# Performance work log

Hardware: AMD Instinct MI355X
Metric: run time of the kernel (lower is better)

Reference implementation:

```python
import jax, jax.numpy as jnp
import numpy as np

NUM_EMB = 512
EMB_DIM = 64

def conv1d(x, w, b=None, stride=1, padding=0):
    # x: (N,C,L), w: (O,I,K) torch Conv1d layout
    out = jax.lax.conv_general_dilated(x, w, (stride,), [(padding, padding)],
                                       dimension_numbers=('NCH', 'OIH', 'NCH'))
    if b is not None:
        out = out + b[None, :, None]
    return out

def conv_transpose1d(x, w, b, stride, padding):
    # w: (I,O,K) torch ConvTranspose1d layout -> flip kernel, swap I/O
    k = w.shape[2]
    wf = jnp.flip(w, 2).transpose(1, 0, 2)  # (O,I,K)
    pad = k - 1 - padding
    out = jax.lax.conv_general_dilated(x, wf, (1,), [(pad, pad)],
                                       lhs_dilation=(stride,),
                                       dimension_numbers=('NCH', 'OIH', 'NCH'))
    return out + b[None, :, None]

def residual_block(x, w1, w2):
    # ReLU -> conv3(pad1, no bias) -> ReLU -> conv1(no bias), residual add
    h = conv1d(jax.nn.relu(x), w1, None, 1, 1)
    h = conv1d(jax.nn.relu(h), w2, None, 1, 0)
    return x + h

def residual_stack(x, r0_w1, r0_w2, r1_w1, r1_w2):
    x = residual_block(x, r0_w1, r0_w2)
    x = residual_block(x, r1_w1, r1_w2)
    return jax.nn.relu(x)

def vq(z, emb):
    # z: (B, C=64, T); torch VectorQuantizerEMA eval path (decay=0, not training)
    B, C, T = z.shape
    inputs = z.transpose(0, 2, 1)                 # (B,T,C)
    flat = inputs.reshape(-1, C)                  # (B*T, C)
    d = (jnp.sum(flat * flat, axis=1, keepdims=True)
         + jnp.sum(emb * emb, axis=1)
         - 2.0 * flat @ emb.T)                    # (B*T, K)
    idx = jnp.argmin(d, axis=1)
    enc = jax.nn.one_hot(idx, NUM_EMB, dtype=flat.dtype)  # (B*T, K)
    q = (enc @ emb).reshape(B, T, C)
    # straight-through estimator
    q = inputs + jax.lax.stop_gradient(q - inputs)
    return q.transpose(0, 2, 1)                   # (B,C,T)

def reference(x, enc_w1, enc_b1, enc_w2, enc_b2, enc_w3, enc_b3,
              enc_r0_w1, enc_r0_w2, enc_r1_w1, enc_r1_w2,
              prevq_w, prevq_b, emb,
              dec_w1, dec_b1, dec_r0_w1, dec_r0_w2, dec_r1_w1, dec_r1_w2,
              dect1_w, dect1_b, dect2_w, dect2_b):
    # Encoder
    h = jax.nn.relu(conv1d(x, enc_w1, enc_b1, 2, 1))
    h = jax.nn.relu(conv1d(h, enc_w2, enc_b2, 2, 1))
    h = conv1d(h, enc_w3, enc_b3, 1, 1)
    h = residual_stack(h, enc_r0_w1, enc_r0_w2, enc_r1_w1, enc_r1_w2)
    # pre-VQ 1x1 conv
    z = conv1d(h, prevq_w, prevq_b, 1, 0)
    # Vector quantization
    q = vq(z, emb)
    # Decoder
    d = conv1d(q, dec_w1, dec_b1, 1, 1)
    d = residual_stack(d, dec_r0_w1, dec_r0_w2, dec_r1_w1, dec_r1_w2)
    d = jax.nn.relu(conv_transpose1d(d, dect1_w, dect1_b, 2, 1))
    return conv_transpose1d(d, dect2_w, dect2_b, 2, 1)

def setup_inputs() -> dict:
    key = jax.random.key(0)
    ks = jax.random.split(key, 25)
    def n(k, shape, s=0.05):
        return jax.random.normal(k, shape, dtype=jnp.float32) * s
    return {
        'x': jax.random.normal(ks[0], (16, 768, 4096), dtype=jnp.float32),
        'enc_w1': n(ks[1], (32, 768, 4)), 'enc_b1': n(ks[2], (32,)),
        'enc_w2': n(ks[3], (64, 32, 4)), 'enc_b2': n(ks[4], (64,)),
        'enc_w3': n(ks[5], (64, 64, 3)), 'enc_b3': n(ks[6], (64,)),
        'enc_r0_w1': n(ks[7], (32, 64, 3)), 'enc_r0_w2': n(ks[8], (64, 32, 1)),
        'enc_r1_w1': n(ks[9], (32, 64, 3)), 'enc_r1_w2': n(ks[10], (64, 32, 1)),
        'prevq_w': n(ks[11], (64, 64, 1)), 'prevq_b': n(ks[12], (64,)),
        'emb': jax.random.normal(ks[13], (512, 64), dtype=jnp.float32),
        'dec_w1': n(ks[14], (64, 64, 3)), 'dec_b1': n(ks[15], (64,)),
        'dec_r0_w1': n(ks[16], (32, 64, 3)), 'dec_r0_w2': n(ks[17], (64, 32, 1)),
        'dec_r1_w1': n(ks[18], (32, 64, 3)), 'dec_r1_w2': n(ks[19], (64, 32, 1)),
        'dect1_w': n(ks[20], (64, 32, 4)), 'dect1_b': n(ks[21], (32,)),
        'dect2_w': n(ks[22], (32, 64, 4)), 'dect2_b': n(ks[23], (64,)),
    }
```

## Files before the change

### kernel.cpp

```cpp
#include <hip/hip_runtime.h>


typedef _Float16 half8 __attribute__((ext_vector_type(8)));
typedef float f32x4 __attribute__((ext_vector_type(4)));
union H8u { half8 h; int4 i; };
union P4u { _Float16 e[4]; int2 u; };

__device__ __forceinline__ void splitf(float v, _Float16& h, _Float16& l) {
  h = (_Float16)v; l = (_Float16)((v - (float)h) * 2048.0f);
}
#define INV2048 (1.0f / 2048.0f)

#define OFF_C1   0
#define OFF_C2   98304
#define OFF_C3   106496
#define OFF_ER0A 122880
#define OFF_ER0B 131072
#define OFF_ER1A 133120
#define OFF_ER1B 141312
#define OFF_PQ   143360
#define OFF_DW1  147456
#define OFF_DR0A 163840
#define OFF_DR0B 172032
#define OFF_DR1A 174080
#define OFF_DR1B 182272
#define OFF_T1   184320
#define OFF_T2   200704
#define WTOT     217088

struct WPtrs {
  const float *c1, *c2, *c3, *er0a, *er0b, *er1a, *er1b, *pq,
              *dw1, *dr0a, *dr0b, *dr1a, *dr1b, *t1, *t2;
};

__device__ __forceinline__ int tpose_kt(int par, int tap) {
  if (par == 0) { if (tap == 0) return 3; if (tap == 1) return 1; }
  else          { if (tap == 1) return 2; if (tap == 2) return 0; }
  return -1;
}

__global__ __launch_bounds__(256) void prep_k(WPtrs P, _Float16* __restrict__ WH,
                                              _Float16* __restrict__ WL) {
  int s = blockIdx.x * 256 + threadIdx.x;
  if (s >= WTOT) return;
  float v = 0.f;
  if (s < OFF_C2) {
    int t = s, co = t / 3072, kk = t % 3072;
    v = P.c1[(co * 768 + (kk >> 2)) * 4 + (kk & 3)];
  } else if (s < OFF_C3) {
    int t = s - OFF_C2, co = t >> 7, kk = t & 127;
    v = P.c2[(co * 32 + (kk >> 2)) * 4 + (kk & 3)];
  } else if (s < OFF_ER0A) {
    int t = s - OFF_C3, co = t >> 8, kk = t & 255, tap = kk & 3;
    if (tap < 3) v = P.c3[(co * 64 + (kk >> 2)) * 3 + tap];
  } else if (s < OFF_ER0B) {
    int t = s - OFF_ER0A, co = t >> 8, kk = t & 255, tap = kk & 3;
    if (tap < 3) v = P.er0a[(co * 64 + (kk >> 2)) * 3 + tap];
  } else if (s < OFF_ER1A) {
    int t = s - OFF_ER0B; v = P.er0b[t];
  } else if (s < OFF_ER1B) {
    int t = s - OFF_ER1A, co = t >> 8, kk = t & 255, tap = kk & 3;
    if (tap < 3) v = P.er1a[(co * 64 + (kk >> 2)) * 3 + tap];
  } else if (s < OFF_PQ) {
    int t = s - OFF_ER1B; v = P.er1b[t];
  } else if (s < OFF_DW1) {
    int t = s - OFF_PQ; v = P.pq[t];
  } else if (s < OFF_DR0A) {
    int t = s - OFF_DW1, co = t >> 8, kk = t & 255, tap = kk & 3;
    if (tap < 3) v = P.dw1[(co * 64 + (kk >> 2)) * 3 + tap];
  } else if (s < OFF_DR0B) {
    int t = s - OFF_DR0A, co = t >> 8, kk = t & 255, tap = kk & 3;
    if (tap < 3) v = P.dr0a[(co * 64 + (kk >> 2)) * 3 + tap];
  } else if (s < OFF_DR1A) {
    int t = s - OFF_DR0B; v = P.dr0b[t];
  } else if (s < OFF_DR1B) {
    int t = s - OFF_DR1A, co = t >> 8, kk = t & 255, tap = kk & 3;
    if (tap < 3) v = P.dr1a[(co * 64 + (kk >> 2)) * 3 + tap];
  } else if (s < OFF_T1) {
    int t = s - OFF_DR1B; v = P.dr1b[t];
  } else if (s < OFF_T2) {
    int t = s - OFF_T1, nn = t >> 8, kk = t & 255;
    int par = nn >> 5, co = nn & 31, ci = kk >> 2;
    int kt = tpose_kt(par, kk & 3);
    if (kt >= 0) v = P.t1[(ci * 32 + co) * 4 + kt];
  } else {
    int t = s - OFF_T2, nn = t >> 7, kk = t & 127;
    int par = nn >> 6, co = nn & 63, ci = kk >> 2;
    int kt = tpose_kt(par, kk & 3);
    if (kt >= 0) v = P.t2[(ci * 64 + co) * 4 + kt];
  }
  _Float16 h, l; splitf(v, h, l);
  WH[s] = h; WL[s] = l;
}

__global__ __launch_bounds__(256, 2) void conv1_k(
    const float* __restrict__ x, const _Float16* __restrict__ WH,
    const _Float16* __restrict__ WL, const float* __restrict__ bias,
    float* __restrict__ out) {
  const int tid = threadIdx.x;
  const int w = tid >> 6, lane = tid & 63, lm = lane & 15, quad = lane >> 4;
  const int m0 = blockIdx.x * 64, n = blockIdx.y;
  const int mrow = m0 + w * 16 + lm;
  const int pbase = 2 * mrow - 1;
  const bool lo = pbase >= 0;
  const bool hi = pbase + 3 <= 4095;
  const int pc0 = lo ? pbase : 1;
  const int pc3 = hi ? pbase + 3 : pbase + 1;
  const float* xn = x + (size_t)n * 768 * 4096;
  const float* xq = xn + (size_t)(quad * 2) * 4096;
  const _Float16* bh0 = WH + (size_t)lm * 3072 + quad * 8;
  const _Float16* bl0 = WL + (size_t)lm * 3072 + quad * 8;
  const _Float16* bh1 = bh0 + 16 * 3072;
  const _Float16* bl1 = bl0 + 16 * 3072;
  f32x4 acc1[2], acc2[2];
#pragma unroll
  for (int j = 0; j < 2; ++j)
#pragma unroll
    for (int r = 0; r < 4; ++r) { acc1[j][r] = 0.f; acc2[j][r] = 0.f; }

#pragma unroll 1
  for (int c = 0; c < 24; ++c) {
    const float* rpc = xq + (size_t)c * 32 * 4096;
    const int kb = c * 128;
#pragma unroll
    for (int ks = 0; ks < 4; ++ks) {
      const float* r0 = rpc + (size_t)ks * 8 * 4096;
      const float* r1 = r0 + 4096;
      float  t0  = r0[pc0];
      float2 v0m = *(const float2*)(r0 + pbase + 1);
      float  t3  = r0[pc3];
      float  u0  = r1[pc0];
      float2 v1m = *(const float2*)(r1 + pbase + 1);
      float  u3  = r1[pc3];
      H8u b0h, b0l, b1h, b1l;
      b0h.i = *(const int4*)(bh0 + kb + ks * 32);
      b0l.i = *(const int4*)(bl0 + kb + ks * 32);
      b1h.i = *(const int4*)(bh1 + kb + ks * 32);
      b1l.i = *(const int4*)(bl1 + kb + ks * 32);
      float a[8];
      a[0] = lo ? t0 : 0.f; a[1] = v0m.x; a[2] = v0m.y; a[3] = hi ? t3 : 0.f;
      a[4] = lo ? u0 : 0.f; a[5] = v1m.x; a[6] = v1m.y; a[7] = hi ? u3 : 0.f;
      H8u ah, al;
#pragma unroll
      for (int e = 0; e < 8; ++e) {
        _Float16 h, l; splitf(a[e], h, l);
        ah.h[e] = h; al.h[e] = l;
      }
      acc1[0] = __builtin_amdgcn_mfma_f32_16x16x32_f16(ah.h, b0h.h, acc1[0], 0, 0, 0);
      acc2[0] = __builtin_amdgcn_mfma_f32_16x16x32_f16(ah.h, b0l.h, acc2[0], 0, 0, 0);
      acc2[0] = __builtin_amdgcn_mfma_f32_16x16x32_f16(al.h, b0h.h, acc2[0], 0, 0, 0);
      acc1[1] = __builtin_amdgcn_mfma_f32_16x16x32_f16(ah.h, b1h.h, acc1[1], 0, 0, 0);
      acc2[1] = __builtin_amdgcn_mfma_f32_16x16x32_f16(ah.h, b1l.h, acc2[1], 0, 0, 0);
      acc2[1] = __builtin_amdgcn_mfma_f32_16x16x32_f16(al.h, b1h.h, acc2[1], 0, 0, 0);
    }
  }
#pragma unroll
  for (int j = 0; j < 2; ++j) {
    int col = j * 16 + lm;
    float bv = bias[col];
    float4 o;
    o.x = fmaxf(acc1[j][0] + acc2[j][0] * INV2048 + bv, 0.f);
    o.y = fmaxf(acc1[j][1] + acc2[j][1] * INV2048 + bv, 0.f);
    o.z = fmaxf(acc1[j][2] + acc2[j][2] * INV2048 + bv, 0.f);
    o.w = fmaxf(acc1[j][3] + acc2[j][3] * INV2048 + bv, 0.f);
    *(float4*)(out + ((size_t)n * 32 + col) * 2048 + m0 + w * 16 + quad * 4) = o;
  }
}

template<int CI, int KP, int NT, int STRIDE,
         bool RELU_IN, bool RELU_OUT, bool BIAS, bool TPOSE, bool RESBLK>
__global__ __launch_bounds__(256) void gconv(
    const float* __restrict__ in, const _Float16* __restrict__ WH,
    const _Float16* __restrict__ WL, const float* __restrict__ bias,
    const _Float16* __restrict__ W2H, const _Float16* __restrict__ W2L,
    float* __restrict__ out, int Lin, int Lout) {
  constexpr int CP = 32 * STRIDE + 4;
  constexpr int CP4 = CP / 4;
  constexpr int AP = KP + 8;
  constexpr int KS = KP / 32;
  constexpr int NTW = (NT == 2) ? 1 : NT / 2;
  __shared__ float xs[CI * CP];
  __shared__ _Float16 Ah[32 * AP];
  __shared__ _Float16 Al[32 * AP];
  __shared__ _Float16 A2h[RESBLK ? 32 * 40 : 1];
  __shared__ _Float16 A2l[RESBLK ? 32 * 40 : 1];
  const int tid = threadIdx.x;
  const int w = tid >> 6, lane = tid & 63, lm = lane & 15, quad = lane >> 4;
  const int mt = w >> 1, ntb = (w & 1) * NTW;
  const int m0 = blockIdx.x * 32, n = blockIdx.y;
  const int base = m0 * STRIDE - 1;
  const float* inN = in + (size_t)n * CI * Lin;
  constexpr int SLOTS = CI * CP4;
#pragma unroll
  for (int it = 0; it < (SLOTS + 255) / 256; ++it) {
    int idx = it * 256 + tid;
    if (idx < SLOTS) {
      int row = idx / CP4, c4 = idx % CP4;
      int p0 = base + c4 * 4;
      const float* rp = inN + (size_t)row * Lin;
      float4 v;
      if (p0 >= 0 && p0 + 3 < Lin) v = *(const float4*)(rp + p0);
      else {
        v.x = (p0   >= 0 && p0   < Lin) ? rp[p0]   : 0.f;
        v.y = (p0+1 >= 0 && p0+1 < Lin) ? rp[p0+1] : 0.f;
        v.z = (p0+2 >= 0 && p0+2 < Lin) ? rp[p0+2] : 0.f;
        v.w = (p0+3 >= 0 && p0+3 < Lin) ? rp[p0+3] : 0.f;
      }
      *(float4*)(&xs[row * CP + c4 * 4]) = v;
    }
  }
  __syncthreads();
#pragma unroll
  for (int it = 0; it < (32 * CI) / 256; ++it) {
    int slot = it * 256 + tid;
    int ci = slot & (CI - 1), m = slot / CI;
    const float* xr = &xs[ci * CP + STRIDE * m];
    float a0 = xr[0], a1 = xr[1], a2 = xr[2], a3 = xr[3];
    if (RELU_IN) { a0 = fmaxf(a0,0.f); a1 = fmaxf(a1,0.f);
                   a2 = fmaxf(a2,0.f); a3 = fmaxf(a3,0.f); }
    P4u ph, pl;
    splitf(a0, ph.e[0], pl.e[0]); splitf(a1, ph.e[1], pl.e[1]);
    splitf(a2, ph.e[2], pl.e[2]); splitf(a3, ph.e[3], pl.e[3]);
    *(int2*)(&Ah[m * AP + ci * 4]) = ph.u;
    *(int2*)(&Al[m * AP + ci * 4]) = pl.u;
  }
  __syncthreads();
  f32x4 acc1[NTW], acc2[NTW];
#pragma unroll
  for (int j = 0; j < NTW; ++j)
#pragma unroll
    for (int r = 0; r < 4; ++r) { acc1[j][r] = 0.f; acc2[j][r] = 0.f; }
  H8u bh[2][NTW], bl[2][NTW];
#pragma unroll
  for (int j = 0; j < NTW; ++j) {
    int col = (ntb + j) * 16 + lm;
    bh[0][j].i = *(const int4*)(WH + (size_t)col * KP + quad * 8);
    bl[0][j].i = *(const int4*)(WL + (size_t)col * KP + quad * 8);
  }
#pragma unroll
  for (int ks = 0; ks < KS; ++ks) {
    int cur = ks & 1;
    if (ks + 1 < KS) {
#pragma unroll
      for (int j = 0; j < NTW; ++j) {
        int col = (ntb + j) * 16 + lm;
        bh[cur ^ 1][j].i = *(const int4*)(WH + (size_t)col * KP + (ks+1) * 32 + quad * 8);
        bl[cur ^ 1][j].i = *(const int4*)(WL + (size_t)col * KP + (ks+1) * 32 + quad * 8);
      }
    }
    H8u ah, al;
    ah.i = *(const int4*)(&Ah[(mt * 16 + lm) * AP + ks * 32 + quad * 8]);
    al.i = *(const int4*)(&Al[(mt * 16 + lm) * AP + ks * 32 + quad * 8]);
#pragma unroll
    for (int j = 0; j < NTW; ++j) {
      acc1[j] = __builtin_amdgcn_mfma_f32_16x16x32_f16(ah.h, bh[cur][j].h, acc1[j], 0,0,0);
      acc2[j] = __builtin_amdgcn_mfma_f32_16x16x32_f16(ah.h, bl[cur][j].h, acc2[j], 0,0,0);
      acc2[j] = __builtin_amdgcn_mfma_f32_16x16x32_f16(al.h, bh[cur][j].h, acc2[j], 0,0,0);
    }
  }
  if (RESBLK) {
    int co2 = (w & 1) * 16 + lm;
#pragma unroll
    for (int r = 0; r < 4; ++r) {
      float hv = fmaxf(acc1[0][r] + acc2[0][r] * INV2048, 0.f);
      _Float16 hh, hl; splitf(hv, hh, hl);
      int m = mt * 16 + quad * 4 + r;
      A2h[m * 40 + co2] = hh; A2l[m * 40 + co2] = hl;
    }
    __syncthreads();
    f32x4 c1[2], c2[2];
#pragma unroll
    for (int j = 0; j < 2; ++j)
#pragma unroll
      for (int r = 0; r < 4; ++r) { c1[j][r] = 0.f; c2[j][r] = 0.f; }
    H8u a2h, a2l;
    a2h.i = *(const int4*)(&A2h[(mt * 16 + lm) * 40 + quad * 8]);
    a2l.i = *(const int4*)(&A2l[(mt * 16 + lm) * 40 + quad * 8]);
    int ntb2 = (w & 1) * 2;
#pragma unroll
    for (int j = 0; j < 2; ++j) {
      int col = (ntb2 + j) * 16 + lm;
      H8u wbh, wbl;
      wbh.i = *(const int4*)(W2H + col * 32 + quad * 8);
      wbl.i = *(const int4*)(W2L + col * 32 + quad * 8);
      c1[j] = __builtin_amdgcn_mfma_f32_16x16x32_f16(a2h.h, wbh.h, c1[j], 0,0,0);
      c2[j] = __builtin_amdgcn_mfma_f32_16x16x32_f16(a2h.h, wbl.h, c2[j], 0,0,0);
      c2[j] = __builtin_amdgcn_mfma_f32_16x16x32_f16(a2l.h, wbh.h, c2[j], 0,0,0);
    }
#pragma unroll
    for (int j = 0; j < 2; ++j) {
      int col = (ntb2 + j) * 16 + lm;
      float4 o;
#pragma unroll
      for (int r = 0; r < 4; ++r) {
        int m = mt * 16 + quad * 4 + r;
        float res = xs[col * CP + m + 1];
        ((float*)&o)[r] = res + c1[j][r] + c2[j][r] * INV2048;
      }
      *(float4*)(out + ((size_t)n * 64 + col) * Lout + m0 + mt * 16 + quad * 4) = o;
    }
  } else {
    constexpr int CO = TPOSE ? NT * 8 : NT * 16;
#pragma unroll
    for (int j = 0; j < NTW; ++j) {
      int col = (ntb + j) * 16 + lm;
      int par = TPOSE ? (col / CO) : 0;
      int co  = TPOSE ? (col % CO) : col;
      float bv = BIAS ? bias[co] : 0.f;
      float vr[4];
#pragma unroll
      for (int r = 0; r < 4; ++r) {
        float v = acc1[j][r] + acc2[j][r] * INV2048 + bv;
        vr[r] = RELU_OUT ? fmaxf(v, 0.f) : v;
      }
      if (TPOSE) {
#pragma unroll
        for (int r = 0; r < 4; ++r) {
          int m = m0 + mt * 16 + quad * 4 + r;
          out[((size_t)n * CO + co) * Lout + 2 * m + par] = vr[r];
        }
      } else {
        float4 o; o.x = vr[0]; o.y = vr[1]; o.z = vr[2]; o.w = vr[3];
        *(float4*)(out + ((size_t)n * CO + co) * Lout + m0 + mt * 16 + quad * 4) = o;
      }
    }
  }
}

__global__ void enorm_k(const float* __restrict__ emb, float* __restrict__ en) {
  int e = blockIdx.x * blockDim.x + threadIdx.x;
  if (e >= 512) return;
  float s = 0.f;
  const float* r = emb + (size_t)e * 64;
  for (int c = 0; c < 64; ++c) s = fmaf(r[c], r[c], s);
  en[e] = s;
}

__global__ __launch_bounds__(256) void vq_fused(
    const float* __restrict__ sIn, const _Float16* __restrict__ PQH,
    const _Float16* __restrict__ PQL, const float* __restrict__ pqb,
    const float* __restrict__ emb, const float* __restrict__ en,
    float* __restrict__ q) {
  __shared__ float xs[64 * 68];
  __shared__ _Float16 Ah[64 * 72];
  __shared__ _Float16 Al[64 * 72];
  __shared__ float zl[64 * 65];
  __shared__ float dred[4 * 64];
  __shared__ int   ired[4 * 64];
  __shared__ int   idxs[64];
  const int tid = threadIdx.x;
  const int w = tid >> 6, lane = tid & 63, lm = lane & 15, quad = lane >> 4;
  const int n = blockIdx.y, t0 = blockIdx.x * 64;
#pragma unroll
  for (int it = 0; it < 4; ++it) {
    int idx = it * 256 + tid;
    int row = idx >> 4, c4 = idx & 15;
    float4 v = *(const float4*)(sIn + ((size_t)n * 64 + row) * 1024 + t0 + c4 * 4);
    *(float4*)(&xs[row * 68 + c4 * 4]) = v;
  }
  __syncthreads();
#pragma unroll
  for (int it = 0; it < 16; ++it) {
    int slot = it * 256 + tid;
    int ci = slot & 63, t = slot >> 6;
    float v = fmaxf(xs[ci * 68 + t], 0.f);
    _Float16 h, l; splitf(v, h, l);
    Ah[t * 72 + ci] = h; Al[t * 72 + ci] = l;
  }
  __syncthreads();
  f32x4 a1[4], a2[4];
#pragma unroll
  for (int j = 0; j < 4; ++j)
#pragma unroll
    for (int r = 0; r < 4; ++r) { a1[j][r] = 0.f; a2[j][r] = 0.f; }
#pragma unroll
  for (int ks = 0; ks < 2; ++ks) {
    H8u ah, al;
    ah.i = *(const int4*)(&Ah[(w * 16 + lm) * 72 + ks * 32 + quad * 8]);
    al.i = *(const int4*)(&Al[(w * 16 + lm) * 72 + ks * 32 + quad * 8]);
#pragma unroll
    for (int j = 0; j < 4; ++j) {
      int col = j * 16 + lm;
      H8u bh, bl;
      bh.i = *(const int4*)(PQH + col * 64 + ks * 32 + quad * 8);
      bl.i = *(const int4*)(PQL + col * 64 + ks * 32 + quad * 8);
      a1[j] = __builtin_amdgcn_mfma_f32_16x16x32_f16(ah.h, bh.h, a1[j], 0,0,0);
      a2[j] = __builtin_amdgcn_mfma_f32_16x16x32_f16(ah.h, bl.h, a2[j], 0,0,0);
      a2[j] = __builtin_amdgcn_mfma_f32_16x16x32_f16(al.h, bh.h, a2[j], 0,0,0);
    }
  }
#pragma unroll
  for (int j = 0; j < 4; ++j) {
    int col = j * 16 + lm;
    float bv = pqb[col];
#pragma unroll
    for (int r = 0; r < 4; ++r) {
      int t = w * 16 + quad * 4 + r;
      zl[t * 65 + col] = a1[j][r] + a2[j][r] * INV2048 + bv;
    }
  }
  __syncthreads();
  int tt = tid & 63, cq = tid >> 6;
  float zv[64];
#pragma unroll
  for (int c = 0; c < 64; ++c) zv[c] = zl[tt * 65 + c];
  float best = 1e30f; int bidx = 0;
  for (int e = cq * 128; e < cq * 128 + 128; ++e) {
    const float* er = emb + (size_t)e * 64;
    float dot = 0.f;
#pragma unroll
    for (int c = 0; c < 64; ++c) dot = fmaf(zv[c], er[c], dot);
    float d = en[e] - 2.f * dot;
    if (d < best) { best = d; bidx = e; }
  }
  dred[cq * 64 + tt] = best;
  ired[cq * 64 + tt] = bidx;
  __syncthreads();
  if (cq == 0) {
    for (int j = 1; j < 4; ++j) {
      float d = dred[j * 64 + tt]; int i2 = ired[j * 64 + tt];
      if (d < best || (d == best && i2 < bidx)) { best = d; bidx = i2; }
    }
    idxs[tt] = bidx;
  }
  __syncthreads();
  for (int it = 0; it < 16; ++it) {
    int c = cq * 16 + it;
    q[((size_t)n * 64 + c) * 1024 + t0 + tt] = emb[(size_t)idxs[tt] * 64 + c];
  }
}

extern "C" void kernel_launch(void* const* d_in, const int* in_sizes, int n_in,
                              void* d_out, int out_size, void* d_ws, size_t ws_size,
                              hipStream_t stream) {
  const float* x        = (const float*)d_in[0];
  const float* enc_b1   = (const float*)d_in[2];
  const float* enc_b2   = (const float*)d_in[4];
  const float* enc_b3   = (const float*)d_in[6];
  const float* prevq_b  = (const float*)d_in[12];
  const float* emb      = (const float*)d_in[13];
  const float* dec_b1   = (const float*)d_in[15];
  const float* dect1_b  = (const float*)d_in[21];
  const float* dect2_b  = (const float*)d_in[23];
  float* out = (float*)d_out;

  WPtrs P;
  P.c1  = (const float*)d_in[1];  P.c2  = (const float*)d_in[3];
  P.c3  = (const float*)d_in[5];  P.er0a = (const float*)d_in[7];
  P.er0b = (const float*)d_in[8]; P.er1a = (const float*)d_in[9];
  P.er1b = (const float*)d_in[10]; P.pq = (const float*)d_in[11];
  P.dw1 = (const float*)d_in[14]; P.dr0a = (const float*)d_in[16];
  P.dr0b = (const float*)d_in[17]; P.dr1a = (const float*)d_in[18];
  P.dr1b = (const float*)d_in[19]; P.t1 = (const float*)d_in[20];
  P.t2  = (const float*)d_in[22];

  float* A  = (float*)d_ws;
  float* B  = A + (1u << 20);
  float* EN = B + (1u << 20);
  _Float16* WH = (_Float16*)(EN + 1024);
  _Float16* WL = WH + WTOT;

  dim3 blk(256);
  prep_k<<<dim3((WTOT + 255) / 256), blk, 0, stream>>>(P, WH, WL);
  enorm_k<<<dim3(2), blk, 0, stream>>>(emb, EN);
  conv1_k<<<dim3(32, 16), blk, 0, stream>>>(x, WH + OFF_C1, WL + OFF_C1, enc_b1, A);
  gconv<32,128,4,2, false,true,true, false,false><<<dim3(32,16), blk, 0, stream>>>(
      A, WH+OFF_C2, WL+OFF_C2, enc_b2, nullptr, nullptr, B, 2048, 1024);
  gconv<64,256,4,1, false,false,true, false,false><<<dim3(32,16), blk, 0, stream>>>(
      B, WH+OFF_C3, WL+OFF_C3, enc_b3, nullptr, nullptr, A, 1024, 1024);
  gconv<64,256,2,1, true,false,false, false,true><<<dim3(32,16), blk, 0, stream>>>(
      A, WH+OFF_ER0A, WL+OFF_ER0A, nullptr, WH+OFF_ER0B, WL+OFF_ER0B, B, 1024, 1024);
  gconv<64,256,2,1, true,false,false, false,true><<<dim3(32,16), blk, 0, stream>>>(
      B, WH+OFF_ER1A, WL+OFF_ER1A, nullptr, WH+OFF_ER1B, WL+OFF_ER1B, A, 1024, 1024);
  vq_fused<<<dim3(16,16), blk, 0, stream>>>(A, WH+OFF_PQ, WL+OFF_PQ, prevq_b, emb, EN, B);
  gconv<64,256,4,1, false,false,true, false,false><<<dim3(32,16), blk, 0, stream>>>(
      B, WH+OFF_DW1, WL+OFF_DW1, dec_b1, nullptr, nullptr, A, 1024, 1024);
  gconv<64,256,2,1, true,false,false, false,true><<<dim3(32,16), blk, 0, stream>>>(
      A, WH+OFF_DR0A, WL+OFF_DR0A, nullptr, WH+OFF_DR0B, WL+OFF_DR0B, B, 1024, 1024);
  gconv<64,256,2,1, true,false,false, false,true><<<dim3(32,16), blk, 0, stream>>>(
      B, WH+OFF_DR1A, WL+OFF_DR1A, nullptr, WH+OFF_DR1B, WL+OFF_DR1B, A, 1024, 1024);
  gconv<64,256,4,1, true,true,true, true,false><<<dim3(32,16), blk, 0, stream>>>(
      A, WH+OFF_T1, WL+OFF_T1, dect1_b, nullptr, nullptr, B, 1024, 2048);
  gconv<32,128,8,1, false,false,true, true,false><<<dim3(64,16), blk, 0, stream>>>(
      B, WH+OFF_T2, WL+OFF_T2, dect2_b, nullptr, nullptr, out, 2048, 4096);
}
```

Before: 643.1 us.

## Split-K the first encoder conv and reduce partials in the next conv

The large first convolution over 768 input channels is split across a new grid z dimension into up to four channel partitions, each writing a partial-sum plane to workspace. The following stride-2 conv sums the partial planes while loading its input tile and applies the first conv's bias and ReLU there. This raises the block count for the memory-heavy first layer to improve occupancy and latency hiding. In exchange it adds extra workspace traffic and depends on the workspace size available.

```diff
diff --git a/kernel.cpp b/kernel.cpp
--- a/kernel.cpp
+++ b/kernel.cpp
@@ -95,11 +95,10 @@
 
 __global__ __launch_bounds__(256, 2) void conv1_k(
     const float* __restrict__ x, const _Float16* __restrict__ WH,
-    const _Float16* __restrict__ WL, const float* __restrict__ bias,
-    float* __restrict__ out) {
+    const _Float16* __restrict__ WL, float* __restrict__ Pout, int cchunks) {
   const int tid = threadIdx.x;
   const int w = tid >> 6, lane = tid & 63, lm = lane & 15, quad = lane >> 4;
-  const int m0 = blockIdx.x * 64, n = blockIdx.y;
+  const int m0 = blockIdx.x * 64, n = blockIdx.y, kpart = blockIdx.z;
   const int mrow = m0 + w * 16 + lm;
   const int pbase = 2 * mrow - 1;
   const bool lo = pbase >= 0;
@@ -118,8 +117,10 @@
 #pragma unroll
     for (int r = 0; r < 4; ++r) { acc1[j][r] = 0.f; acc2[j][r] = 0.f; }
 
+  const int c0 = kpart * cchunks;
 #pragma unroll 1
-  for (int c = 0; c < 24; ++c) {
+  for (int cc = 0; cc < cchunks; ++cc) {
+    const int c = c0 + cc;
     const float* rpc = xq + (size_t)c * 32 * 4096;
     const int kb = c * 128;
 #pragma unroll
@@ -157,23 +158,25 @@
 #pragma unroll
   for (int j = 0; j < 2; ++j) {
     int col = j * 16 + lm;
-    float bv = bias[col];
     float4 o;
-    o.x = fmaxf(acc1[j][0] + acc2[j][0] * INV2048 + bv, 0.f);
-    o.y = fmaxf(acc1[j][1] + acc2[j][1] * INV2048 + bv, 0.f);
-    o.z = fmaxf(acc1[j][2] + acc2[j][2] * INV2048 + bv, 0.f);
-    o.w = fmaxf(acc1[j][3] + acc2[j][3] * INV2048 + bv, 0.f);
-    *(float4*)(out + ((size_t)n * 32 + col) * 2048 + m0 + w * 16 + quad * 4) = o;
+    o.x = acc1[j][0] + acc2[j][0] * INV2048;
+    o.y = acc1[j][1] + acc2[j][1] * INV2048;
+    o.z = acc1[j][2] + acc2[j][2] * INV2048;
+    o.w = acc1[j][3] + acc2[j][3] * INV2048;
+    *(float4*)(Pout + (size_t)kpart * (16 * 32 * 2048)
+               + ((size_t)n * 32 + col) * 2048 + m0 + w * 16 + quad * 4) = o;
   }
 }
 
 template<int CI, int KP, int NT, int STRIDE,
-         bool RELU_IN, bool RELU_OUT, bool BIAS, bool TPOSE, bool RESBLK>
+         bool RELU_IN, bool RELU_OUT, bool BIAS, bool TPOSE, bool RESBLK,
+         bool PSUM = false>
 __global__ __launch_bounds__(256) void gconv(
     const float* __restrict__ in, const _Float16* __restrict__ WH,
     const _Float16* __restrict__ WL, const float* __restrict__ bias,
     const _Float16* __restrict__ W2H, const _Float16* __restrict__ W2L,
-    float* __restrict__ out, int Lin, int Lout) {
+    float* __restrict__ out, int Lin, int Lout,
+    const float* __restrict__ inbias, int nparts, int pplane) {
   constexpr int CP = 32 * STRIDE + 4;
   constexpr int CP4 = CP / 4;
   constexpr int AP = KP + 8;
@@ -199,12 +202,38 @@
       int p0 = base + c4 * 4;
       const float* rp = inN + (size_t)row * Lin;
       float4 v;
-      if (p0 >= 0 && p0 + 3 < Lin) v = *(const float4*)(rp + p0);
-      else {
-        v.x = (p0   >= 0 && p0   < Lin) ? rp[p0]   : 0.f;
-        v.y = (p0+1 >= 0 && p0+1 < Lin) ? rp[p0+1] : 0.f;
-        v.z = (p0+2 >= 0 && p0+2 < Lin) ? rp[p0+2] : 0.f;
-        v.w = (p0+3 >= 0 && p0+3 < Lin) ? rp[p0+3] : 0.f;
+      if (PSUM) {
+        v.x = 0.f; v.y = 0.f; v.z = 0.f; v.w = 0.f;
+        bool i0 = (p0   >= 0 && p0   < Lin);
+        bool i1 = (p0+1 >= 0 && p0+1 < Lin);
+        bool i2 = (p0+2 >= 0 && p0+2 < Lin);
+        bool i3 = (p0+3 >= 0 && p0+3 < Lin);
+        bool full = (p0 >= 0 && p0 + 3 < Lin);
+        for (int p = 0; p < nparts; ++p) {
+          const float* rpp = rp + (size_t)p * pplane;
+          if (full) {
+            float4 t = *(const float4*)(rpp + p0);
+            v.x += t.x; v.y += t.y; v.z += t.z; v.w += t.w;
+          } else {
+            if (i0) v.x += rpp[p0];
+            if (i1) v.y += rpp[p0+1];
+            if (i2) v.z += rpp[p0+2];
+            if (i3) v.w += rpp[p0+3];
+          }
+        }
+        float bv = inbias[row];
+        v.x = i0 ? fmaxf(v.x + bv, 0.f) : 0.f;
+        v.y = i1 ? fmaxf(v.y + bv, 0.f) : 0.f;
+        v.z = i2 ? fmaxf(v.z + bv, 0.f) : 0.f;
+        v.w = i3 ? fmaxf(v.w + bv, 0.f) : 0.f;
+      } else {
+        if (p0 >= 0 && p0 + 3 < Lin) v = *(const float4*)(rp + p0);
+        else {
+          v.x = (p0   >= 0 && p0   < Lin) ? rp[p0]   : 0.f;
+          v.y = (p0+1 >= 0 && p0+1 < Lin) ? rp[p0+1] : 0.f;
+          v.z = (p0+2 >= 0 && p0+2 < Lin) ? rp[p0+2] : 0.f;
+          v.w = (p0+3 >= 0 && p0+3 < Lin) ? rp[p0+3] : 0.f;
+        }
       }
       *(float4*)(&xs[row * CP + c4 * 4]) = v;
     }
@@ -459,28 +488,46 @@
   float* EN = B + (1u << 20);
   _Float16* WH = (_Float16*)(EN + 1024);
   _Float16* WL = WH + WTOT;
+  float* PP = (float*)(WL + WTOT);
+
+  const size_t baseBytes = (size_t)((char*)PP - (char*)d_ws);
+  const size_t planeB = (size_t)16 * 32 * 2048 * 4;
+  int nparts = 1;
+  float* Pbuf = A;
+  if (ws_size >= baseBytes + 4 * planeB) { nparts = 4; Pbuf = PP; }
+  else if (ws_size >= baseBytes + 2 * planeB) { nparts = 2; Pbuf = PP; }
 
   dim3 blk(256);
   prep_k<<<dim3((WTOT + 255) / 256), blk, 0, stream>>>(P, WH, WL);
   enorm_k<<<dim3(2), blk, 0, stream>>>(emb, EN);
-  conv1_k<<<dim3(32, 16), blk, 0, stream>>>(x, WH + OFF_C1, WL + OFF_C1, enc_b1, A);
-  gconv<32,128,4,2, false,true,true, false,false><<<dim3(32,16), blk, 0, stream>>>(
-      A, WH+OFF_C2, WL+OFF_C2, enc_b2, nullptr, nullptr, B, 2048, 1024);
+  conv1_k<<<dim3(32, 16, nparts), blk, 0, stream>>>(x, WH + OFF_C1, WL + OFF_C1,
+                                                    Pbuf, 24 / nparts);
+  gconv<32,128,4,2, false,true,true, false,false, true><<<dim3(32,16), blk, 0, stream>>>(
+      Pbuf, WH+OFF_C2, WL+OFF_C2, enc_b2, nullptr, nullptr, B, 2048, 1024,
+      enc_b1, nparts, 16 * 32 * 2048);
   gconv<64,256,4,1, false,false,true, false,false><<<dim3(32,16), blk, 0, stream>>>(
-      B, WH+OFF_C3, WL+OFF_C3, enc_b3, nullptr, nullptr, A, 1024, 1024);
+      B, WH+OFF_C3, WL+OFF_C3, enc_b3, nullptr, nullptr, A, 1024, 1024,
+      nullptr, 1, 0);
   gconv<64,256,2,1, true,false,false, false,true><<<dim3(32,16), blk, 0, stream>>>(
-      A, WH+OFF_ER0A, WL+OFF_ER0A, nullptr, WH+OFF_ER0B, WL+OFF_ER0B, B, 1024, 1024);
+      A, WH+OFF_ER0A, WL+OFF_ER0A, nullptr, WH+OFF_ER0B, WL+OFF_ER0B, B, 1024, 1024,
+      nullptr, 1, 0);
   gconv<64,256,2,1, true,false,false, false,true><<<dim3(32,16), blk, 0, stream>>>(
-      B, WH+OFF_ER1A, WL+OFF_ER1A, nullptr, WH+OFF_ER1B, WL+OFF_ER1B, A, 1024, 1024);
+      B, WH+OFF_ER1A, WL+OFF_ER1A, nullptr, WH+OFF_ER1B, WL+OFF_ER1B, A, 1024, 1024,
+      nullptr, 1, 0);
   vq_fused<<<dim3(16,16), blk, 0, stream>>>(A, WH+OFF_PQ, WL+OFF_PQ, prevq_b, emb, EN, B);
   gconv<64,256,4,1, false,false,true, false,false><<<dim3(32,16), blk, 0, stream>>>(
-      B, WH+OFF_DW1, WL+OFF_DW1, dec_b1, nullptr, nullptr, A, 1024, 1024);
+      B, WH+OFF_DW1, WL+OFF_DW1, dec_b1, nullptr, nullptr, A, 1024, 1024,
+      nullptr, 1, 0);
   gconv<64,256,2,1, true,false,false, false,true><<<dim3(32,16), blk, 0, stream>>>(
-      A, WH+OFF_DR0A, WL+OFF_DR0A, nullptr, WH+OFF_DR0B, WL+OFF_DR0B, B, 1024, 1024);
+      A, WH+OFF_DR0A, WL+OFF_DR0A, nullptr, WH+OFF_DR0B, WL+OFF_DR0B, B, 1024, 1024,
+      nullptr, 1, 0);
   gconv<64,256,2,1, true,false,false, false,true><<<dim3(32,16), blk, 0, stream>>>(
-      B, WH+OFF_DR1A, WL+OFF_DR1A, nullptr, WH+OFF_DR1B, WL+OFF_DR1B, A, 1024, 1024);
+      B, WH+OFF_DR1A, WL+OFF_DR1A, nullptr, WH+OFF_DR1B, WL+OFF_DR1B, A, 1024, 1024,
+      nullptr, 1, 0);
   gconv<64,256,4,1, true,true,true, true,false><<<dim3(32,16), blk, 0, stream>>>(
-      A, WH+OFF_T1, WL+OFF_T1, dect1_b, nullptr, nullptr, B, 1024, 2048);
+      A, WH+OFF_T1, WL+OFF_T1, dect1_b, nullptr, nullptr, B, 1024, 2048,
+      nullptr, 1, 0);
   gconv<32,128,8,1, false,false,true, true,false><<<dim3(64,16), blk, 0, stream>>>(
-      B, WH+OFF_T2, WL+OFF_T2, dect2_b, nullptr, nullptr, out, 2048, 4096);
-}
+      B, WH+OFF_T2, WL+OFF_T2, dect2_b, nullptr, nullptr, out, 2048, 4096,
+      nullptr, 1, 0);
+}
```

Result: no change. 633.2 us (-1.5%).
